# Optimization experiments

Hardware: AMD Instinct MI355X
Metric: run time of the kernel (lower is better)

## Reference

```python
import jax, jax.numpy as jnp
import numpy as np

B, S, D, H = 2, 2048, 1024, 16
DK = D // H


def setup_inputs() -> dict:
    key = jax.random.key(0)
    ks = jax.random.split(key, 7)
    x = jax.random.normal(ks[0], (B, S, D), dtype=jnp.float32)
    gamma = jax.random.normal(ks[1], (D,), dtype=jnp.float32)
    mask = jax.random.randint(ks[2], (B, S), 0, 2, dtype=jnp.int32)
    w_qkv_w = jax.random.normal(ks[3], (D, 3 * D), dtype=jnp.float32) / np.sqrt(D)
    w_qkv_b = jax.random.normal(ks[4], (3 * D,), dtype=jnp.float32) * 0.02
    w_o_w = jax.random.normal(ks[5], (D, D), dtype=jnp.float32) / np.sqrt(D)
    w_o_b = jax.random.normal(ks[6], (D,), dtype=jnp.float32) * 0.02
    return {"x": x, "gamma": gamma, "mask": mask, "w_qkv_w": w_qkv_w,
            "w_qkv_b": w_qkv_b, "w_o_w": w_o_w, "w_o_b": w_o_b}


def reference(x, gamma, mask, w_qkv_w, w_qkv_b, w_o_w, w_o_b):
    b, s, d = x.shape
    # QKV projection, then per-head interleaved chunk (matches torch view+chunk)
    qkv = x @ w_qkv_w + w_qkv_b                      # [B,S,3D]
    qkv = qkv.reshape(b, s, H, 3 * DK).transpose(0, 2, 1, 3)  # [B,H,S,3*dk]
    q, k, v = jnp.split(qkv, 3, axis=-1)             # each [B,H,S,dk]
    scale = 1.0 / np.sqrt(DK).astype(np.float32)
    scores = jnp.einsum('bhqd,bhkd->bhqk', q, k) * scale  # [B,H,S,S]
    m = mask[:, None, None, :]                       # 2D mask -> [B,1,1,S]
    scores = jnp.where(m == 0, -jnp.inf, scores)
    attn = jax.nn.softmax(scores, axis=-1)           # dropout p=0.0 -> identity
    out = jnp.einsum('bhqk,bhkd->bhqd', attn, v)     # [B,H,S,dk]
    out = out.transpose(0, 2, 1, 3).reshape(b, s, d) # [B,S,D]
    out = out @ w_o_w + w_o_b
    return (gamma + 1.0) * out
```

## Files before the change

kernel.cpp:

```cpp
#include <hip/hip_runtime.h>
#include <hip/hip_bf16.h>


using bf16 = __hip_bfloat16;
typedef __attribute__((ext_vector_type(8))) short bf16x8;
typedef __attribute__((ext_vector_type(4))) float f32x4;

#define QSCALE 0.18033688011112042f

static __device__ __forceinline__ f32x4 mfma_bf16(bf16x8 a, bf16x8 b, f32x4 c) {
    return __builtin_amdgcn_mfma_f32_16x16x32_bf16(a, b, c, 0, 0, 0);
}

static __device__ __forceinline__ void gld_lds16(const void* g, void* s) {
    __builtin_amdgcn_global_load_lds(
        (const __attribute__((address_space(1))) unsigned int*)g,
        (__attribute__((address_space(3))) unsigned int*)s,
        16, 0, 0);
}

static __device__ __forceinline__ short f2s(float f) {
    bf16 h = __float2bfloat16(f);
    return *reinterpret_cast<short*>(&h);
}

__global__ void prep_kernel(const float* __restrict__ x, bf16* __restrict__ xb,
                            const float* __restrict__ wqkv, bf16* __restrict__ wqkvT,
                            const float* __restrict__ wo, bf16* __restrict__ woT) {
    __shared__ float tile[32][33];
    int blk = blockIdx.x;
    if (blk < 4096) {
        int i = blk * 256 + threadIdx.x;
        float4 f = reinterpret_cast<const float4*>(x)[i];
        xb[4*i+0] = __float2bfloat16(f.x);
        xb[4*i+1] = __float2bfloat16(f.y);
        xb[4*i+2] = __float2bfloat16(f.z);
        xb[4*i+3] = __float2bfloat16(f.w);
        return;
    }
    const float* in; bf16* out; int R, C, bx, by;
    if (blk < 7168) {
        int idx = blk - 4096; in = wqkv; out = wqkvT; R = 1024; C = 3072;
        bx = idx % 96; by = idx / 96;
    } else {
        int idx = blk - 7168; in = wo; out = woT; R = 1024; C = 1024;
        bx = idx & 31; by = idx >> 5;
    }
    int c0 = bx * 32, r0 = by * 32;
    int xo = threadIdx.x & 31, yo = threadIdx.x >> 5;
#pragma unroll
    for (int i = 0; i < 32; i += 8) tile[yo + i][xo] = in[(size_t)(r0 + yo + i) * C + c0 + xo];
    __syncthreads();
#pragma unroll
    for (int i = 0; i < 32; i += 8)
        out[(size_t)(c0 + yo + i) * R + r0 + xo] = __float2bfloat16(tile[xo][yo + i]);
}

template <int TM, int MINW>
__global__ __launch_bounds__(256, MINW)
void gemm_bt_kernel(const bf16* __restrict__ A, const bf16* __restrict__ Bt,
                    int M, int N, int K,
                    const float* __restrict__ bias,
                    bf16* __restrict__ Qout, bf16* __restrict__ Kout, bf16* __restrict__ Vout) {
    constexpr int MI = TM / 32;
    constexpr int CA = TM / 32;
    __shared__ __align__(16) bf16 As[TM * 64];
    __shared__ __align__(16) bf16 Bs[128 * 64];

    const int tid  = threadIdx.x;
    const int wave = tid >> 6, lane = tid & 63;
    const int quad = lane >> 4, l16 = lane & 15;
    const int wr = wave >> 1, wc = wave & 1;
    const int bm = blockIdx.y, bn = blockIdx.x;

    f32x4 acc[MI][4] = {};

    const int crow = lane >> 3;
    const int sblk = (lane & 7) ^ (crow & 7);
    const bf16* gA[CA]; const bf16* gB[4]; bf16* lA[CA]; bf16* lB[4];
#pragma unroll
    for (int c = 0; c < CA; ++c) {
        int ch = wave * CA + c;
        gA[c] = A + (size_t)(bm * TM + ch * 8 + crow) * K + sblk * 8;
        lA[c] = As + ch * 512 + lane * 8;
    }
#pragma unroll
    for (int c = 0; c < 4; ++c) {
        int ch = wave * 4 + c;
        gB[c] = Bt + (size_t)(bn * 128 + ch * 8 + crow) * K + sblk * 8;
        lB[c] = Bs + ch * 512 + lane * 8;
    }
    const int xr = l16 & 7;

    for (int k0 = 0; k0 < K; k0 += 64) {
#pragma unroll
        for (int c = 0; c < CA; ++c) gld_lds16(gA[c] + k0, lA[c]);
#pragma unroll
        for (int c = 0; c < 4; ++c) gld_lds16(gB[c] + k0, lB[c]);
        __syncthreads();
#pragma unroll
        for (int ks = 0; ks < 2; ++ks) {
            bf16x8 af[MI], bfr[4];
#pragma unroll
            for (int mi = 0; mi < MI; ++mi)
                af[mi] = *(const bf16x8*)(As + (wr * (TM/2) + mi * 16 + l16) * 64 + ((4 * ks + quad) ^ xr) * 8);
#pragma unroll
            for (int ni = 0; ni < 4; ++ni)
                bfr[ni] = *(const bf16x8*)(Bs + (wc * 64 + ni * 16 + l16) * 64 + ((4 * ks + quad) ^ xr) * 8);
#pragma unroll
            for (int mi = 0; mi < MI; ++mi)
#pragma unroll
                for (int ni = 0; ni < 4; ++ni)
                    acc[mi][ni] = mfma_bf16(af[mi], bfr[ni], acc[mi][ni]);
        }
        __syncthreads();
    }

#pragma unroll
    for (int mi = 0; mi < MI; ++mi) {
#pragma unroll
        for (int ni = 0; ni < 4; ++ni) {
            const int col = bn * 128 + wc * 64 + ni * 16 + l16;
            const int row0 = bm * TM + wr * (TM/2) + mi * 16 + quad * 4;
            const float bs = bias[col];
            float vv[4];
#pragma unroll
            for (int r = 0; r < 4; ++r) vv[r] = acc[mi][ni][r] + bs;
            const int h = col / 192;
            const int rr = col - h * 192;
            const int which = rr >> 6, dk = rr & 63;
            const int b = row0 >> 11, s0 = row0 & 2047;
            const size_t bh = (size_t)b * 16 + h;
            if (which == 0) {
#pragma unroll
                for (int r = 0; r < 4; ++r)
                    Qout[(bh * 2048 + s0 + r) * 64 + dk] = __float2bfloat16(vv[r] * QSCALE);
            } else if (which == 1) {
#pragma unroll
                for (int r = 0; r < 4; ++r)
                    Kout[(bh * 2048 + s0 + r) * 64 + dk] = __float2bfloat16(vv[r]);
            } else {
                const int sp0 = (s0 & ~31) | ((s0 & 12) << 1) | ((s0 & 16) >> 2);
                short4 pv;
                pv.x = f2s(vv[0]); pv.y = f2s(vv[1]);
                pv.z = f2s(vv[2]); pv.w = f2s(vv[3]);
                *reinterpret_cast<short4*>(&Vout[(bh * 64 + dk) * 2048 + sp0]) = pv;
            }
        }
    }
}

__global__ __launch_bounds__(512, 2)
void gemm_out_kernel(const bf16* __restrict__ A, const bf16* __restrict__ Bt,
                     const float* __restrict__ bias, const float* __restrict__ gamma,
                     float* __restrict__ Cout) {
    constexpr int K = 1024, N = 1024;
    __shared__ __align__(16) bf16 As[128 * 64];
    __shared__ __align__(16) bf16 Bs[128 * 64];

    const int tid = threadIdx.x;
    const int wave = tid >> 6, lane = tid & 63;
    const int quad = lane >> 4, l16 = lane & 15;
    const int wr = wave >> 1, wc = wave & 1;

    const int lid = blockIdx.x + (blockIdx.y << 3);
    const int w = (lid & 7) * 32 + (lid >> 3);
    const int bm = w >> 3, bn = w & 7;

    f32x4 acc[2][4] = {};

    const int crow = lane >> 3;
    const int sblk = (lane & 7) ^ (crow & 7);
    const bf16* gA[2]; const bf16* gB[2]; bf16* lA[2]; bf16* lB[2];
#pragma unroll
    for (int c = 0; c < 2; ++c) {
        int ch = wave * 2 + c;
        gA[c] = A + (size_t)(bm * 128 + ch * 8 + crow) * K + sblk * 8;
        lA[c] = As + ch * 512 + lane * 8;
        gB[c] = Bt + (size_t)(bn * 128 + ch * 8 + crow) * K + sblk * 8;
        lB[c] = Bs + ch * 512 + lane * 8;
    }
    const int xr = l16 & 7;

    for (int k0 = 0; k0 < K; k0 += 64) {
#pragma unroll
        for (int c = 0; c < 2; ++c) {
            gld_lds16(gA[c] + k0, lA[c]);
            gld_lds16(gB[c] + k0, lB[c]);
        }
        __syncthreads();
#pragma unroll
        for (int ks = 0; ks < 2; ++ks) {
            bf16x8 af[2], bfr[4];
#pragma unroll
            for (int mi = 0; mi < 2; ++mi)
                af[mi] = *(const bf16x8*)(As + (wr * 32 + mi * 16 + l16) * 64 + ((4 * ks + quad) ^ xr) * 8);
#pragma unroll
            for (int ni = 0; ni < 4; ++ni)
                bfr[ni] = *(const bf16x8*)(Bs + (wc * 64 + ni * 16 + l16) * 64 + ((4 * ks + quad) ^ xr) * 8);
#pragma unroll
            for (int mi = 0; mi < 2; ++mi)
#pragma unroll
                for (int ni = 0; ni < 4; ++ni)
                    acc[mi][ni] = mfma_bf16(af[mi], bfr[ni], acc[mi][ni]);
        }
        __syncthreads();
    }

#pragma unroll
    for (int mi = 0; mi < 2; ++mi)
#pragma unroll
        for (int ni = 0; ni < 4; ++ni) {
            const int col = bn * 128 + wc * 64 + ni * 16 + l16;
            const int row0 = bm * 128 + wr * 32 + mi * 16 + quad * 4;
            const float bs = bias[col];
            const float gm = gamma[col] + 1.0f;
#pragma unroll
            for (int r = 0; r < 4; ++r)
                Cout[(size_t)(row0 + r) * N + col] = gm * (acc[mi][ni][r] + bs);
        }
}

__global__ __launch_bounds__(256, 2)
void attn_kernel(const bf16* __restrict__ Qb, const bf16* __restrict__ Kb,
                 const bf16* __restrict__ Vtp, const int* __restrict__ mask,
                 bf16* __restrict__ Aout) {
    __shared__ __align__(16) bf16 Ks[2][2][4096];
    __shared__ __align__(16) bf16 Vs[2][2][4096];
    __shared__ float Biass[2][2][64];

    const int lid = blockIdx.x + (blockIdx.y << 4);
    const int w   = (lid & 7) * 64 + (lid >> 3);
    const int bh  = w >> 4;
    const int b = bh >> 4, h = bh & 15;
    const int q0 = (w & 15) * 128;
    const int tid = threadIdx.x;
    const int wave = tid >> 6, lane = tid & 63;
    const int qg = wave >> 1, kg = wave & 1;
    const int quad = lane >> 4, l16 = lane & 15;
    const int xr = l16 & 7;

    bf16x8 aq[4][2];
#pragma unroll
    for (int m = 0; m < 4; ++m) {
        const bf16* qp = Qb + ((size_t)bh * 2048 + q0 + qg * 64 + m * 16 + l16) * 64;
        aq[m][0] = *(const bf16x8*)(qp + quad * 8);
        aq[m][1] = *(const bf16x8*)(qp + 32 + quad * 8);
    }

    bf16x8 ones;
#pragma unroll
    for (int j = 0; j < 8; ++j) ones[j] = (short)0x3F80;

    f32x4 O[4][4] = {};
    f32x4 Lacc[4] = {};

    const int r8 = lane >> 3, b8 = lane & 7;
    const int srcb = b8 ^ r8;
    const bf16* gK = Kb  + ((size_t)bh * 2048 + wave * 8 + r8) * 64 + srcb * 8;
    const bf16* gV = Vtp + ((size_t)bh * 64 + wave * 8 + r8) * 2048 + srcb * 8;
    const int so = wave * 512 + lane * 8;

    int mreg = 0;
#pragma unroll
    for (int ti = 0; ti < 2; ++ti)
#pragma unroll
        for (int c = 0; c < 2; ++c) {
            gld_lds16(gK + (size_t)ti * 4096 + c * 2048, &Ks[0][ti][c * 2048 + so]);
            gld_lds16(gV + (size_t)ti * 64 + c * 65536, &Vs[0][ti][c * 2048 + so]);
        }
    if (tid < 128) {
        Biass[0][tid >> 6][tid & 63] = mask[b * 2048 + tid] ? -24.0f : -1e30f;
        mreg = mask[b * 2048 + 128 + tid];
    }

    for (int t = 0; t < 16; ++t) {
        __syncthreads();
        const int cur = t & 1, nxt = cur ^ 1;

        if (t < 15) {
            const int u0 = 2 * t + 2;
#pragma unroll
            for (int ti = 0; ti < 2; ++ti)
#pragma unroll
                for (int c = 0; c < 2; ++c) {
                    gld_lds16(gK + (size_t)(u0 + ti) * 4096 + c * 2048, &Ks[nxt][ti][c * 2048 + so]);
                    gld_lds16(gV + (size_t)(u0 + ti) * 64 + c * 65536, &Vs[nxt][ti][c * 2048 + so]);
                }
            if (tid < 128) Biass[nxt][tid >> 6][tid & 63] = mreg ? -24.0f : -1e30f;
        }
        if (t < 14 && tid < 128) mreg = mask[b * 2048 + t * 128 + 256 + tid];

        const bf16* kb = &Ks[cur][kg][0];
        const bf16* vb = &Vs[cur][kg][0];
        f32x4 bias4[4];
        bf16x8 bk[4][2];
#pragma unroll
        for (int kt4 = 0; kt4 < 4; ++kt4) {
            bias4[kt4] = *(const f32x4*)(&Biass[cur][kg][0] + kt4 * 16 + quad * 4);
            const bf16* kp2 = kb + (kt4 * 16 + l16) * 64;
            bk[kt4][0] = *(const bf16x8*)(kp2 + (quad ^ xr) * 8);
            bk[kt4][1] = *(const bf16x8*)(kp2 + ((quad + 4) ^ xr) * 8);
        }
        bf16x8 bv[2][4];
#pragma unroll
        for (int a = 0; a < 2; ++a)
#pragma unroll
            for (int nt = 0; nt < 4; ++nt)
                bv[a][nt] = *(const bf16x8*)(vb + (nt * 16 + l16) * 64 + ((a * 4 + quad) ^ xr) * 8);

        f32x4 sv0[2][4], sv1[2][4];
        __builtin_amdgcn_s_setprio(1);
#pragma unroll
        for (int mm = 0; mm < 2; ++mm)
#pragma unroll
            for (int kt4 = 0; kt4 < 4; ++kt4) {
                f32x4 c = mfma_bf16(bk[kt4][0], aq[mm][0], bias4[kt4]);
                sv0[mm][kt4] = mfma_bf16(bk[kt4][1], aq[mm][1], c);
            }

#pragma unroll
        for (int kt4 = 0; kt4 < 4; ++kt4) {
            f32x4 c0 = mfma_bf16(bk[kt4][0], aq[2][0], bias4[kt4]);
#pragma unroll
            for (int r = 0; r < 4; ++r)
                sv0[0][kt4][r] = __builtin_amdgcn_exp2f(sv0[0][kt4][r]);
            f32x4 c1 = mfma_bf16(bk[kt4][0], aq[3][0], bias4[kt4]);
#pragma unroll
            for (int r = 0; r < 4; ++r)
                sv0[1][kt4][r] = __builtin_amdgcn_exp2f(sv0[1][kt4][r]);
            sv1[0][kt4] = mfma_bf16(bk[kt4][1], aq[2][1], c0);
            sv1[1][kt4] = mfma_bf16(bk[kt4][1], aq[3][1], c1);
        }

#pragma unroll
        for (int mm = 0; mm < 2; ++mm) {
#pragma unroll
            for (int a = 0; a < 2; ++a) {
                bf16x8 pa;
                pa[0] = f2s(sv0[mm][2*a][0]);   pa[1] = f2s(sv0[mm][2*a][1]);
                pa[2] = f2s(sv0[mm][2*a][2]);   pa[3] = f2s(sv0[mm][2*a][3]);
                pa[4] = f2s(sv0[mm][2*a+1][0]); pa[5] = f2s(sv0[mm][2*a+1][1]);
                pa[6] = f2s(sv0[mm][2*a+1][2]); pa[7] = f2s(sv0[mm][2*a+1][3]);
                Lacc[mm] = mfma_bf16(pa, ones, Lacc[mm]);
#pragma unroll
                for (int nt = 0; nt < 4; ++nt)
                    O[mm][nt] = mfma_bf16(pa, bv[a][nt], O[mm][nt]);
#pragma unroll
                for (int r = 0; r < 4; ++r)
                    sv1[mm][2*a + (r >> 1)][(r & 1) + 2*((mm + a) & 1)] =
                        __builtin_amdgcn_exp2f(sv1[mm][2*a + (r >> 1)][(r & 1) + 2*((mm + a) & 1)]);
            }
        }
#pragma unroll
        for (int mm = 0; mm < 2; ++mm)
#pragma unroll
            for (int a = 0; a < 2; ++a)
#pragma unroll
                for (int r = 0; r < 4; ++r) {
                    int kt4 = 2*a + (r >> 1);
                    int ri  = (r & 1) + 2*(((mm + a) & 1) ^ 1);
                    sv1[mm][kt4][ri] = __builtin_amdgcn_exp2f(sv1[mm][kt4][ri]);
                }

#pragma unroll
        for (int mm = 0; mm < 2; ++mm) {
            const int m = 2 + mm;
#pragma unroll
            for (int a = 0; a < 2; ++a) {
                bf16x8 pa;
                pa[0] = f2s(sv1[mm][2*a][0]);   pa[1] = f2s(sv1[mm][2*a][1]);
                pa[2] = f2s(sv1[mm][2*a][2]);   pa[3] = f2s(sv1[mm][2*a][3]);
                pa[4] = f2s(sv1[mm][2*a+1][0]); pa[5] = f2s(sv1[mm][2*a+1][1]);
                pa[6] = f2s(sv1[mm][2*a+1][2]); pa[7] = f2s(sv1[mm][2*a+1][3]);
                Lacc[m] = mfma_bf16(pa, ones, Lacc[m]);
#pragma unroll
                for (int nt = 0; nt < 4; ++nt)
                    O[m][nt] = mfma_bf16(pa, bv[a][nt], O[m][nt]);
            }
        }
        __builtin_amdgcn_s_setprio(0);
    }

    __syncthreads();
    float* cb = (float*)&Ks[0][0][0];
    float* lb = (float*)&Vs[0][0][0];
    if (kg == 1) {
#pragma unroll
        for (int m = 0; m < 4; ++m) {
#pragma unroll
            for (int nt = 0; nt < 4; ++nt)
#pragma unroll
                for (int r = 0; r < 4; ++r)
                    cb[qg * 4096 + (m * 16 + nt * 4 + r) * 64 + lane] = O[m][nt][r];
#pragma unroll
            for (int r = 0; r < 4; ++r)
                lb[qg * 1024 + (m * 4 + r) * 64 + lane] = Lacc[m][r];
        }
    }
    __syncthreads();
    if (kg == 0) {
#pragma unroll
        for (int m = 0; m < 4; ++m) {
            float inv[4];
#pragma unroll
            for (int r = 0; r < 4; ++r)
                inv[r] = __builtin_amdgcn_rcpf(Lacc[m][r] + lb[qg * 1024 + (m * 4 + r) * 64 + lane]);
#pragma unroll
            for (int nt = 0; nt < 4; ++nt)
#pragma unroll
                for (int r = 0; r < 4; ++r) {
                    int row = q0 + qg * 64 + m * 16 + quad * 4 + r;
                    float o = O[m][nt][r] + cb[qg * 4096 + (m * 16 + nt * 4 + r) * 64 + lane];
                    Aout[((size_t)b * 2048 + row) * 1024 + h * 64 + nt * 16 + l16] =
                        __float2bfloat16(o * inv[r]);
                }
        }
    }
}

extern "C" void kernel_launch(void* const* d_in, const int* in_sizes, int n_in,
                              void* d_out, int out_size, void* d_ws, size_t ws_size,
                              hipStream_t stream) {
    const float* x     = (const float*)d_in[0];
    const float* gamma = (const float*)d_in[1];
    const int*   mask  = (const int*)d_in[2];
    const float* wqkv  = (const float*)d_in[3];
    const float* bqkv  = (const float*)d_in[4];
    const float* wo    = (const float*)d_in[5];
    const float* bo    = (const float*)d_in[6];
    float* out = (float*)d_out;

    char* ws = (char*)d_ws;
    const size_t MB = 1u << 20;
    bf16* xb    = (bf16*)(ws);
    bf16* wqkvT = (bf16*)(ws + 8 * MB);
    bf16* woT   = (bf16*)(ws + 14 * MB);
    bf16* Qb    = (bf16*)(ws + 16 * MB);
    bf16* Kb    = (bf16*)(ws + 24 * MB);
    bf16* Vt    = (bf16*)(ws + 32 * MB);
    bf16* attn  = (bf16*)(ws + 40 * MB);

    prep_kernel<<<8192, 256, 0, stream>>>(x, xb, wqkv, wqkvT, wo, woT);

    gemm_bt_kernel<128, 3><<<dim3(24, 32), 256, 0, stream>>>(
        xb, wqkvT, 4096, 3072, 1024, bqkv, Qb, Kb, Vt);

    attn_kernel<<<dim3(16, 32), 256, 0, stream>>>(Qb, Kb, Vt, mask, attn);

    gemm_out_kernel<<<dim3(8, 32), 512, 0, stream>>>(attn, woT, bo, gamma, out);
}
```

Before: 173.8 us.

## Fuse attention and output projection into one kernel with a grid barrier

Merges the attention kernel and the output-projection GEMM into a single persistent launch of 512 blocks. An atomic-counter grid barrier, reset by the prep kernel, separates the attention phase from the GEMM phase. The GEMM phase reuses the attention LDS and switches to 64x128 tiles computed by 256 threads. This removes one kernel launch and its tail, but relies on all 512 blocks being co-resident (two per CU), risks deadlock if occupancy falls short, and adds barrier spin cost.

```diff
diff --git a/kernel.cpp b/kernel.cpp
--- a/kernel.cpp
+++ b/kernel.cpp
@@ -24,11 +24,24 @@
     return *reinterpret_cast<short*>(&h);
 }
 
+static __device__ __forceinline__ void grid_sync(unsigned* bar, unsigned nblk) {
+    __syncthreads();
+    if (threadIdx.x == 0) {
+        __threadfence();
+        atomicAdd(bar, 1u);
+        while (atomicAdd(bar, 0u) < nblk) __builtin_amdgcn_s_sleep(2);
+        __threadfence();
+    }
+    __syncthreads();
+}
+
 __global__ void prep_kernel(const float* __restrict__ x, bf16* __restrict__ xb,
                             const float* __restrict__ wqkv, bf16* __restrict__ wqkvT,
-                            const float* __restrict__ wo, bf16* __restrict__ woT) {
+                            const float* __restrict__ wo, bf16* __restrict__ woT,
+                            unsigned* __restrict__ bar) {
     __shared__ float tile[32][33];
     int blk = blockIdx.x;
+    if (blk == 0 && threadIdx.x == 0) atomicExch(bar, 0u);
     if (blk < 4096) {
         int i = blk * 256 + threadIdx.x;
         float4 f = reinterpret_cast<const float4*>(x)[i];
@@ -150,272 +163,272 @@
     }
 }
 
-__global__ __launch_bounds__(512, 2)
-void gemm_out_kernel(const bf16* __restrict__ A, const bf16* __restrict__ Bt,
-                     const float* __restrict__ bias, const float* __restrict__ gamma,
-                     float* __restrict__ Cout) {
-    constexpr int K = 1024, N = 1024;
-    __shared__ __align__(16) bf16 As[128 * 64];
-    __shared__ __align__(16) bf16 Bs[128 * 64];
-
+__global__ __launch_bounds__(256, 2)
+void attn_out_kernel(const bf16* __restrict__ Qb, const bf16* __restrict__ Kb,
+                     const bf16* __restrict__ Vtp, const int* __restrict__ mask,
+                     bf16* __restrict__ Aout,
+                     const bf16* __restrict__ WoT, const float* __restrict__ bo,
+                     const float* __restrict__ gamma, float* __restrict__ Cout,
+                     unsigned* __restrict__ bar) {
+    __shared__ __align__(16) bf16 Ks[2][2][4096];
+    __shared__ __align__(16) bf16 Vs[2][2][4096];
+    __shared__ float Biass[2][2][64];
+
+    const int lid = blockIdx.x + (blockIdx.y << 4);
     const int tid = threadIdx.x;
     const int wave = tid >> 6, lane = tid & 63;
     const int quad = lane >> 4, l16 = lane & 15;
-    const int wr = wave >> 1, wc = wave & 1;
-
-    const int lid = blockIdx.x + (blockIdx.y << 3);
-    const int w = (lid & 7) * 32 + (lid >> 3);
-    const int bm = w >> 3, bn = w & 7;
-
-    f32x4 acc[2][4] = {};
-
-    const int crow = lane >> 3;
-    const int sblk = (lane & 7) ^ (crow & 7);
-    const bf16* gA[2]; const bf16* gB[2]; bf16* lA[2]; bf16* lB[2];
-#pragma unroll
-    for (int c = 0; c < 2; ++c) {
-        int ch = wave * 2 + c;
-        gA[c] = A + (size_t)(bm * 128 + ch * 8 + crow) * K + sblk * 8;
-        lA[c] = As + ch * 512 + lane * 8;
-        gB[c] = Bt + (size_t)(bn * 128 + ch * 8 + crow) * K + sblk * 8;
-        lB[c] = Bs + ch * 512 + lane * 8;
-    }
     const int xr = l16 & 7;
 
-    for (int k0 = 0; k0 < K; k0 += 64) {
+    {
+        const int w   = (lid & 7) * 64 + (lid >> 3);
+        const int bh  = w >> 4;
+        const int b = bh >> 4, h = bh & 15;
+        const int q0 = (w & 15) * 128;
+        const int qg = (wave >> 1) & 1, kg = wave & 1;
+
+        bf16x8 aq[4][2];
+#pragma unroll
+        for (int m = 0; m < 4; ++m) {
+            const bf16* qp = Qb + ((size_t)bh * 2048 + q0 + qg * 64 + m * 16 + l16) * 64;
+            aq[m][0] = *(const bf16x8*)(qp + quad * 8);
+            aq[m][1] = *(const bf16x8*)(qp + 32 + quad * 8);
+        }
+
+        bf16x8 ones;
+#pragma unroll
+        for (int j = 0; j < 8; ++j) ones[j] = (short)0x3F80;
+
+        f32x4 O[4][4] = {};
+        f32x4 Lacc[4] = {};
+
+        const int r8 = lane >> 3, b8 = lane & 7;
+        const int srcb = b8 ^ r8;
+        const bf16* gK = Kb  + ((size_t)bh * 2048 + wave * 8 + r8) * 64 + srcb * 8;
+        const bf16* gV = Vtp + ((size_t)bh * 64 + wave * 8 + r8) * 2048 + srcb * 8;
+        const int so = wave * 512 + lane * 8;
+
+        int mreg = 0;
+#pragma unroll
+        for (int ti = 0; ti < 2; ++ti)
+#pragma unroll
+            for (int c = 0; c < 2; ++c) {
+                gld_lds16(gK + (size_t)ti * 4096 + c * 2048, &Ks[0][ti][c * 2048 + so]);
+                gld_lds16(gV + (size_t)ti * 64 + c * 65536, &Vs[0][ti][c * 2048 + so]);
+            }
+        if (tid < 128) {
+            Biass[0][tid >> 6][tid & 63] = mask[b * 2048 + tid] ? -24.0f : -1e30f;
+            mreg = mask[b * 2048 + 128 + tid];
+        }
+
+        for (int t = 0; t < 16; ++t) {
+            __syncthreads();
+            const int cur = t & 1, nxt = cur ^ 1;
+
+            if (t < 15) {
+                const int u0 = 2 * t + 2;
+#pragma unroll
+                for (int ti = 0; ti < 2; ++ti)
+#pragma unroll
+                    for (int c = 0; c < 2; ++c) {
+                        gld_lds16(gK + (size_t)(u0 + ti) * 4096 + c * 2048, &Ks[nxt][ti][c * 2048 + so]);
+                        gld_lds16(gV + (size_t)(u0 + ti) * 64 + c * 65536, &Vs[nxt][ti][c * 2048 + so]);
+                    }
+                if (tid < 128) Biass[nxt][tid >> 6][tid & 63] = mreg ? -24.0f : -1e30f;
+            }
+            if (t < 14 && tid < 128) mreg = mask[b * 2048 + t * 128 + 256 + tid];
+
+            const bf16* kb = &Ks[cur][kg][0];
+            const bf16* vb = &Vs[cur][kg][0];
+            f32x4 bias4[4];
+            bf16x8 bk[4][2];
+#pragma unroll
+            for (int kt4 = 0; kt4 < 4; ++kt4) {
+                bias4[kt4] = *(const f32x4*)(&Biass[cur][kg][0] + kt4 * 16 + quad * 4);
+                const bf16* kp2 = kb + (kt4 * 16 + l16) * 64;
+                bk[kt4][0] = *(const bf16x8*)(kp2 + (quad ^ xr) * 8);
+                bk[kt4][1] = *(const bf16x8*)(kp2 + ((quad + 4) ^ xr) * 8);
+            }
+            bf16x8 bv[2][4];
+#pragma unroll
+            for (int a = 0; a < 2; ++a)
+#pragma unroll
+                for (int nt = 0; nt < 4; ++nt)
+                    bv[a][nt] = *(const bf16x8*)(vb + (nt * 16 + l16) * 64 + ((a * 4 + quad) ^ xr) * 8);
+
+            f32x4 sv0[2][4], sv1[2][4];
+            __builtin_amdgcn_s_setprio(1);
+#pragma unroll
+            for (int mm = 0; mm < 2; ++mm)
+#pragma unroll
+                for (int kt4 = 0; kt4 < 4; ++kt4) {
+                    f32x4 c = mfma_bf16(bk[kt4][0], aq[mm][0], bias4[kt4]);
+                    sv0[mm][kt4] = mfma_bf16(bk[kt4][1], aq[mm][1], c);
+                }
+
+#pragma unroll
+            for (int kt4 = 0; kt4 < 4; ++kt4) {
+                f32x4 c0 = mfma_bf16(bk[kt4][0], aq[2][0], bias4[kt4]);
+#pragma unroll
+                for (int r = 0; r < 4; ++r)
+                    sv0[0][kt4][r] = __builtin_amdgcn_exp2f(sv0[0][kt4][r]);
+                f32x4 c1 = mfma_bf16(bk[kt4][0], aq[3][0], bias4[kt4]);
+#pragma unroll
+                for (int r = 0; r < 4; ++r)
+                    sv0[1][kt4][r] = __builtin_amdgcn_exp2f(sv0[1][kt4][r]);
+                sv1[0][kt4] = mfma_bf16(bk[kt4][1], aq[2][1], c0);
+                sv1[1][kt4] = mfma_bf16(bk[kt4][1], aq[3][1], c1);
+            }
+
+#pragma unroll
+            for (int mm = 0; mm < 2; ++mm) {
+#pragma unroll
+                for (int a = 0; a < 2; ++a) {
+                    bf16x8 pa;
+                    pa[0] = f2s(sv0[mm][2*a][0]);   pa[1] = f2s(sv0[mm][2*a][1]);
+                    pa[2] = f2s(sv0[mm][2*a][2]);   pa[3] = f2s(sv0[mm][2*a][3]);
+                    pa[4] = f2s(sv0[mm][2*a+1][0]); pa[5] = f2s(sv0[mm][2*a+1][1]);
+                    pa[6] = f2s(sv0[mm][2*a+1][2]); pa[7] = f2s(sv0[mm][2*a+1][3]);
+                    Lacc[mm] = mfma_bf16(pa, ones, Lacc[mm]);
+#pragma unroll
+                    for (int nt = 0; nt < 4; ++nt)
+                        O[mm][nt] = mfma_bf16(pa, bv[a][nt], O[mm][nt]);
+#pragma unroll
+                    for (int r = 0; r < 4; ++r)
+                        sv1[mm][2*a + (r >> 1)][(r & 1) + 2*((mm + a) & 1)] =
+                            __builtin_amdgcn_exp2f(sv1[mm][2*a + (r >> 1)][(r & 1) + 2*((mm + a) & 1)]);
+                }
+            }
+#pragma unroll
+            for (int mm = 0; mm < 2; ++mm)
+#pragma unroll
+                for (int a = 0; a < 2; ++a)
+#pragma unroll
+                    for (int r = 0; r < 4; ++r) {
+                        int kt4 = 2*a + (r >> 1);
+                        int ri  = (r & 1) + 2*(((mm + a) & 1) ^ 1);
+                        sv1[mm][kt4][ri] = __builtin_amdgcn_exp2f(sv1[mm][kt4][ri]);
+                    }
+
+#pragma unroll
+            for (int mm = 0; mm < 2; ++mm) {
+                const int m = 2 + mm;
+#pragma unroll
+                for (int a = 0; a < 2; ++a) {
+                    bf16x8 pa;
+                    pa[0] = f2s(sv1[mm][2*a][0]);   pa[1] = f2s(sv1[mm][2*a][1]);
+                    pa[2] = f2s(sv1[mm][2*a][2]);   pa[3] = f2s(sv1[mm][2*a][3]);
+                    pa[4] = f2s(sv1[mm][2*a+1][0]); pa[5] = f2s(sv1[mm][2*a+1][1]);
+                    pa[6] = f2s(sv1[mm][2*a+1][2]); pa[7] = f2s(sv1[mm][2*a+1][3]);
+                    Lacc[m] = mfma_bf16(pa, ones, Lacc[m]);
+#pragma unroll
+                    for (int nt = 0; nt < 4; ++nt)
+                        O[m][nt] = mfma_bf16(pa, bv[a][nt], O[m][nt]);
+                }
+            }
+            __builtin_amdgcn_s_setprio(0);
+        }
+
+        __syncthreads();
+        float* cb = (float*)&Ks[0][0][0];
+        float* lb = (float*)&Vs[0][0][0];
+        if (kg == 1) {
+#pragma unroll
+            for (int m = 0; m < 4; ++m) {
+#pragma unroll
+                for (int nt = 0; nt < 4; ++nt)
+#pragma unroll
+                    for (int r = 0; r < 4; ++r)
+                        cb[qg * 4096 + (m * 16 + nt * 4 + r) * 64 + lane] = O[m][nt][r];
+#pragma unroll
+                for (int r = 0; r < 4; ++r)
+                    lb[qg * 1024 + (m * 4 + r) * 64 + lane] = Lacc[m][r];
+            }
+        }
+        __syncthreads();
+        if (kg == 0) {
+#pragma unroll
+            for (int m = 0; m < 4; ++m) {
+                float inv[4];
+#pragma unroll
+                for (int r = 0; r < 4; ++r)
+                    inv[r] = __builtin_amdgcn_rcpf(Lacc[m][r] + lb[qg * 1024 + (m * 4 + r) * 64 + lane]);
+#pragma unroll
+                for (int nt = 0; nt < 4; ++nt)
+#pragma unroll
+                    for (int r = 0; r < 4; ++r) {
+                        int row = q0 + qg * 64 + m * 16 + quad * 4 + r;
+                        Aout[((size_t)b * 2048 + row) * 1024 + h * 64 + nt * 16 + l16] =
+                            __float2bfloat16((O[m][nt][r] + cb[qg * 4096 + (m * 16 + nt * 4 + r) * 64 + lane]) * inv[r]);
+                    }
+            }
+        }
+    }
+
+    grid_sync(bar, 512u);
+
+    {
+        constexpr int K = 1024, N = 1024;
+        bf16* As_ = &Ks[0][0][0];
+        bf16* Bs_ = &Ks[0][0][0] + 4096;
+
+        const int wr = wave >> 1, wc = wave & 1;
+        const int w3 = (lid & 7) * 64 + (lid >> 3);
+        const int bm = w3 >> 3, bn = w3 & 7;
+
+        f32x4 acc[2][4] = {};
+        const int crow = lane >> 3;
+        const int sblk = (lane & 7) ^ (crow & 7);
+        const bf16* gA[2]; const bf16* gB[4]; bf16* lA[2]; bf16* lB[4];
 #pragma unroll
         for (int c = 0; c < 2; ++c) {
-            gld_lds16(gA[c] + k0, lA[c]);
-            gld_lds16(gB[c] + k0, lB[c]);
-        }
-        __syncthreads();
-#pragma unroll
-        for (int ks = 0; ks < 2; ++ks) {
-            bf16x8 af[2], bfr[4];
-#pragma unroll
-            for (int mi = 0; mi < 2; ++mi)
-                af[mi] = *(const bf16x8*)(As + (wr * 32 + mi * 16 + l16) * 64 + ((4 * ks + quad) ^ xr) * 8);
-#pragma unroll
-            for (int ni = 0; ni < 4; ++ni)
-                bfr[ni] = *(const bf16x8*)(Bs + (wc * 64 + ni * 16 + l16) * 64 + ((4 * ks + quad) ^ xr) * 8);
-#pragma unroll
-            for (int mi = 0; mi < 2; ++mi)
+            int ch = wave * 2 + c;
+            gA[c] = Aout + (size_t)(bm * 64 + ch * 8 + crow) * K + sblk * 8;
+            lA[c] = As_ + ch * 512 + lane * 8;
+        }
+#pragma unroll
+        for (int c = 0; c < 4; ++c) {
+            int ch = wave * 4 + c;
+            gB[c] = WoT + (size_t)(bn * 128 + ch * 8 + crow) * K + sblk * 8;
+            lB[c] = Bs_ + ch * 512 + lane * 8;
+        }
+
+        for (int k0 = 0; k0 < K; k0 += 64) {
+#pragma unroll
+            for (int c = 0; c < 2; ++c) gld_lds16(gA[c] + k0, lA[c]);
+#pragma unroll
+            for (int c = 0; c < 4; ++c) gld_lds16(gB[c] + k0, lB[c]);
+            __syncthreads();
+#pragma unroll
+            for (int ks = 0; ks < 2; ++ks) {
+                bf16x8 af[2], bfr[4];
+#pragma unroll
+                for (int mi = 0; mi < 2; ++mi)
+                    af[mi] = *(const bf16x8*)(As_ + (wr * 32 + mi * 16 + l16) * 64 + ((4 * ks + quad) ^ xr) * 8);
 #pragma unroll
                 for (int ni = 0; ni < 4; ++ni)
-                    acc[mi][ni] = mfma_bf16(af[mi], bfr[ni], acc[mi][ni]);
-        }
-        __syncthreads();
-    }
-
-#pragma unroll
-    for (int mi = 0; mi < 2; ++mi)
-#pragma unroll
-        for (int ni = 0; ni < 4; ++ni) {
-            const int col = bn * 128 + wc * 64 + ni * 16 + l16;
-            const int row0 = bm * 128 + wr * 32 + mi * 16 + quad * 4;
-            const float bs = bias[col];
-            const float gm = gamma[col] + 1.0f;
-#pragma unroll
-            for (int r = 0; r < 4; ++r)
-                Cout[(size_t)(row0 + r) * N + col] = gm * (acc[mi][ni][r] + bs);
-        }
-}
-
-__global__ __launch_bounds__(256, 2)
-void attn_kernel(const bf16* __restrict__ Qb, const bf16* __restrict__ Kb,
-                 const bf16* __restrict__ Vtp, const int* __restrict__ mask,
-                 bf16* __restrict__ Aout) {
-    __shared__ __align__(16) bf16 Ks[2][2][4096];
-    __shared__ __align__(16) bf16 Vs[2][2][4096];
-    __shared__ float Biass[2][2][64];
-
-    const int lid = blockIdx.x + (blockIdx.y << 4);
-    const int w   = (lid & 7) * 64 + (lid >> 3);
-    const int bh  = w >> 4;
-    const int b = bh >> 4, h = bh & 15;
-    const int q0 = (w & 15) * 128;
-    const int tid = threadIdx.x;
-    const int wave = tid >> 6, lane = tid & 63;
-    const int qg = wave >> 1, kg = wave & 1;
-    const int quad = lane >> 4, l16 = lane & 15;
-    const int xr = l16 & 7;
-
-    bf16x8 aq[4][2];
-#pragma unroll
-    for (int m = 0; m < 4; ++m) {
-        const bf16* qp = Qb + ((size_t)bh * 2048 + q0 + qg * 64 + m * 16 + l16) * 64;
-        aq[m][0] = *(const bf16x8*)(qp + quad * 8);
-        aq[m][1] = *(const bf16x8*)(qp + 32 + quad * 8);
-    }
-
-    bf16x8 ones;
-#pragma unroll
-    for (int j = 0; j < 8; ++j) ones[j] = (short)0x3F80;
-
-    f32x4 O[4][4] = {};
-    f32x4 Lacc[4] = {};
-
-    const int r8 = lane >> 3, b8 = lane & 7;
-    const int srcb = b8 ^ r8;
-    const bf16* gK = Kb  + ((size_t)bh * 2048 + wave * 8 + r8) * 64 + srcb * 8;
-    const bf16* gV = Vtp + ((size_t)bh * 64 + wave * 8 + r8) * 2048 + srcb * 8;
-    const int so = wave * 512 + lane * 8;
-
-    int mreg = 0;
-#pragma unroll
-    for (int ti = 0; ti < 2; ++ti)
-#pragma unroll
-        for (int c = 0; c < 2; ++c) {
-            gld_lds16(gK + (size_t)ti * 4096 + c * 2048, &Ks[0][ti][c * 2048 + so]);
-            gld_lds16(gV + (size_t)ti * 64 + c * 65536, &Vs[0][ti][c * 2048 + so]);
-        }
-    if (tid < 128) {
-        Biass[0][tid >> 6][tid & 63] = mask[b * 2048 + tid] ? -24.0f : -1e30f;
-        mreg = mask[b * 2048 + 128 + tid];
-    }
-
-    for (int t = 0; t < 16; ++t) {
-        __syncthreads();
-        const int cur = t & 1, nxt = cur ^ 1;
-
-        if (t < 15) {
-            const int u0 = 2 * t + 2;
-#pragma unroll
-            for (int ti = 0; ti < 2; ++ti)
-#pragma unroll
-                for (int c = 0; c < 2; ++c) {
-                    gld_lds16(gK + (size_t)(u0 + ti) * 4096 + c * 2048, &Ks[nxt][ti][c * 2048 + so]);
-                    gld_lds16(gV + (size_t)(u0 + ti) * 64 + c * 65536, &Vs[nxt][ti][c * 2048 + so]);
-                }
-            if (tid < 128) Biass[nxt][tid >> 6][tid & 63] = mreg ? -24.0f : -1e30f;
-        }
-        if (t < 14 && tid < 128) mreg = mask[b * 2048 + t * 128 + 256 + tid];
-
-        const bf16* kb = &Ks[cur][kg][0];
-        const bf16* vb = &Vs[cur][kg][0];
-        f32x4 bias4[4];
-        bf16x8 bk[4][2];
-#pragma unroll
-        for (int kt4 = 0; kt4 < 4; ++kt4) {
-            bias4[kt4] = *(const f32x4*)(&Biass[cur][kg][0] + kt4 * 16 + quad * 4);
-            const bf16* kp2 = kb + (kt4 * 16 + l16) * 64;
-            bk[kt4][0] = *(const bf16x8*)(kp2 + (quad ^ xr) * 8);
-            bk[kt4][1] = *(const bf16x8*)(kp2 + ((quad + 4) ^ xr) * 8);
-        }
-        bf16x8 bv[2][4];
-#pragma unroll
-        for (int a = 0; a < 2; ++a)
-#pragma unroll
-            for (int nt = 0; nt < 4; ++nt)
-                bv[a][nt] = *(const bf16x8*)(vb + (nt * 16 + l16) * 64 + ((a * 4 + quad) ^ xr) * 8);
-
-        f32x4 sv0[2][4], sv1[2][4];
-        __builtin_amdgcn_s_setprio(1);
-#pragma unroll
-        for (int mm = 0; mm < 2; ++mm)
-#pragma unroll
-            for (int kt4 = 0; kt4 < 4; ++kt4) {
-                f32x4 c = mfma_bf16(bk[kt4][0], aq[mm][0], bias4[kt4]);
-                sv0[mm][kt4] = mfma_bf16(bk[kt4][1], aq[mm][1], c);
-            }
-
-#pragma unroll
-        for (int kt4 = 0; kt4 < 4; ++kt4) {
-            f32x4 c0 = mfma_bf16(bk[kt4][0], aq[2][0], bias4[kt4]);
-#pragma unroll
-            for (int r = 0; r < 4; ++r)
-                sv0[0][kt4][r] = __builtin_amdgcn_exp2f(sv0[0][kt4][r]);
-            f32x4 c1 = mfma_bf16(bk[kt4][0], aq[3][0], bias4[kt4]);
-#pragma unroll
-            for (int r = 0; r < 4; ++r)
-                sv0[1][kt4][r] = __builtin_amdgcn_exp2f(sv0[1][kt4][r]);
-            sv1[0][kt4] = mfma_bf16(bk[kt4][1], aq[2][1], c0);
-            sv1[1][kt4] = mfma_bf16(bk[kt4][1], aq[3][1], c1);
-        }
-
-#pragma unroll
-        for (int mm = 0; mm < 2; ++mm) {
-#pragma unroll
-            for (int a = 0; a < 2; ++a) {
-                bf16x8 pa;
-                pa[0] = f2s(sv0[mm][2*a][0]);   pa[1] = f2s(sv0[mm][2*a][1]);
-                pa[2] = f2s(sv0[mm][2*a][2]);   pa[3] = f2s(sv0[mm][2*a][3]);
-                pa[4] = f2s(sv0[mm][2*a+1][0]); pa[5] = f2s(sv0[mm][2*a+1][1]);
-                pa[6] = f2s(sv0[mm][2*a+1][2]); pa[7] = f2s(sv0[mm][2*a+1][3]);
-                Lacc[mm] = mfma_bf16(pa, ones, Lacc[mm]);
-#pragma unroll
-                for (int nt = 0; nt < 4; ++nt)
-                    O[mm][nt] = mfma_bf16(pa, bv[a][nt], O[mm][nt]);
-#pragma unroll
-                for (int r = 0; r < 4; ++r)
-                    sv1[mm][2*a + (r >> 1)][(r & 1) + 2*((mm + a) & 1)] =
-                        __builtin_amdgcn_exp2f(sv1[mm][2*a + (r >> 1)][(r & 1) + 2*((mm + a) & 1)]);
-            }
-        }
-#pragma unroll
-        for (int mm = 0; mm < 2; ++mm)
-#pragma unroll
-            for (int a = 0; a < 2; ++a)
-#pragma unroll
-                for (int r = 0; r < 4; ++r) {
-                    int kt4 = 2*a + (r >> 1);
-                    int ri  = (r & 1) + 2*(((mm + a) & 1) ^ 1);
-                    sv1[mm][kt4][ri] = __builtin_amdgcn_exp2f(sv1[mm][kt4][ri]);
-                }
-
-#pragma unroll
-        for (int mm = 0; mm < 2; ++mm) {
-            const int m = 2 + mm;
-#pragma unroll
-            for (int a = 0; a < 2; ++a) {
-                bf16x8 pa;
-                pa[0] = f2s(sv1[mm][2*a][0]);   pa[1] = f2s(sv1[mm][2*a][1]);
-                pa[2] = f2s(sv1[mm][2*a][2]);   pa[3] = f2s(sv1[mm][2*a][3]);
-                pa[4] = f2s(sv1[mm][2*a+1][0]); pa[5] = f2s(sv1[mm][2*a+1][1]);
-                pa[6] = f2s(sv1[mm][2*a+1][2]); pa[7] = f2s(sv1[mm][2*a+1][3]);
-                Lacc[m] = mfma_bf16(pa, ones, Lacc[m]);
-#pragma unroll
-                for (int nt = 0; nt < 4; ++nt)
-                    O[m][nt] = mfma_bf16(pa, bv[a][nt], O[m][nt]);
-            }
-        }
-        __builtin_amdgcn_s_setprio(0);
-    }
-
-    __syncthreads();
-    float* cb = (float*)&Ks[0][0][0];
-    float* lb = (float*)&Vs[0][0][0];
-    if (kg == 1) {
-#pragma unroll
-        for (int m = 0; m < 4; ++m) {
-#pragma unroll
-            for (int nt = 0; nt < 4; ++nt)
-#pragma unroll
-                for (int r = 0; r < 4; ++r)
-                    cb[qg * 4096 + (m * 16 + nt * 4 + r) * 64 + lane] = O[m][nt][r];
-#pragma unroll
-            for (int r = 0; r < 4; ++r)
-                lb[qg * 1024 + (m * 4 + r) * 64 + lane] = Lacc[m][r];
-        }
-    }
-    __syncthreads();
-    if (kg == 0) {
-#pragma unroll
-        for (int m = 0; m < 4; ++m) {
-            float inv[4];
-#pragma unroll
-            for (int r = 0; r < 4; ++r)
-                inv[r] = __builtin_amdgcn_rcpf(Lacc[m][r] + lb[qg * 1024 + (m * 4 + r) * 64 + lane]);
-#pragma unroll
-            for (int nt = 0; nt < 4; ++nt)
-#pragma unroll
-                for (int r = 0; r < 4; ++r) {
-                    int row = q0 + qg * 64 + m * 16 + quad * 4 + r;
-                    float o = O[m][nt][r] + cb[qg * 4096 + (m * 16 + nt * 4 + r) * 64 + lane];
-                    Aout[((size_t)b * 2048 + row) * 1024 + h * 64 + nt * 16 + l16] =
-                        __float2bfloat16(o * inv[r]);
-                }
-        }
+                    bfr[ni] = *(const bf16x8*)(Bs_ + (wc * 64 + ni * 16 + l16) * 64 + ((4 * ks + quad) ^ xr) * 8);
+#pragma unroll
+                for (int mi = 0; mi < 2; ++mi)
+#pragma unroll
+                    for (int ni = 0; ni < 4; ++ni)
+                        acc[mi][ni] = mfma_bf16(af[mi], bfr[ni], acc[mi][ni]);
+            }
+            __syncthreads();
+        }
+
+#pragma unroll
+        for (int mi = 0; mi < 2; ++mi)
+#pragma unroll
+            for (int ni = 0; ni < 4; ++ni) {
+                const int col = bn * 128 + wc * 64 + ni * 16 + l16;
+                const int row0 = bm * 64 + wr * 32 + mi * 16 + quad * 4;
+                const float bs = bo[col];
+                const float gm = gamma[col] + 1.0f;
+#pragma unroll
+                for (int r = 0; r < 4; ++r)
+                    Cout[(size_t)(row0 + r) * N + col] = gm * (acc[mi][ni][r] + bs);
+            }
     }
 }
 
@@ -440,13 +453,13 @@
     bf16* Kb    = (bf16*)(ws + 24 * MB);
     bf16* Vt    = (bf16*)(ws + 32 * MB);
     bf16* attn  = (bf16*)(ws + 40 * MB);
-
-    prep_kernel<<<8192, 256, 0, stream>>>(x, xb, wqkv, wqkvT, wo, woT);
+    unsigned* bar = (unsigned*)(ws + 48 * MB);
+
+    prep_kernel<<<8192, 256, 0, stream>>>(x, xb, wqkv, wqkvT, wo, woT, bar);
 
     gemm_bt_kernel<128, 3><<<dim3(24, 32), 256, 0, stream>>>(
         xb, wqkvT, 4096, 3072, 1024, bqkv, Qb, Kb, Vt);
 
-    attn_kernel<<<dim3(16, 32), 256, 0, stream>>>(Qb, Kb, Vt, mask, attn);
-
-    gemm_out_kernel<<<dim3(8, 32), 512, 0, stream>>>(attn, woT, bo, gamma, out);
-}
+    attn_out_kernel<<<dim3(16, 32), 256, 0, stream>>>(
+        Qb, Kb, Vt, mask, attn, woT, bo, gamma, out, bar);
+}
```

Measured after the change: 217.3 us. +25.0%, slower.
